# Optimization experiments

Measured on AMD Instinct MI355X. Metric: run time of the kernel, lower is better.

The kernel has to match this reference:

```python
import jax, jax.numpy as jnp
import numpy as np

B = 4096
V = 778        # MANO mesh vertices
NJ = 16        # kinematic joints
NC = 30        # pose PCA components
NS = 10        # shape components
NF = 1538      # faces
PARENTS = [0, 0, 1, 2, 0, 4, 5, 0, 7, 8, 0, 10, 11, 0, 13, 14]


def rodrigues(r):
    # r: [N,3] axis-angle -> [N,3,3] rotation matrix (Rodrigues formula)
    theta = jnp.sqrt(jnp.sum(r * r, axis=1) + 1e-8)      # [N]
    k = r / theta[:, None]
    zero = jnp.zeros_like(theta)
    K = jnp.stack([zero, -k[:, 2], k[:, 1],
                   k[:, 2], zero, -k[:, 0],
                   -k[:, 1], k[:, 0], zero], axis=1).reshape(-1, 3, 3)
    s = jnp.sin(theta)[:, None, None]
    c = jnp.cos(theta)[:, None, None]
    return jnp.eye(3, dtype=r.dtype) + s * K + (1.0 - c) * jnp.matmul(K, K)


def setup_inputs() -> dict:
    key = jax.random.key(0)
    ks = jax.random.split(key, 11)
    rot = 0.2 * jax.random.normal(ks[0], (B, 3), jnp.float32)
    pose_params = jax.random.normal(ks[1], (B, NC), jnp.float32)
    shape_params = jax.random.normal(ks[2], (B, NS), jnp.float32)
    v_template = 0.01 * jax.random.normal(ks[3], (V, 3), jnp.float32)
    shapedirs = 0.01 * jax.random.normal(ks[4], (V, 3, NS), jnp.float32)
    posedirs = 0.001 * jax.random.normal(ks[5], (V, 3, (NJ - 1) * 9), jnp.float32)
    jr = jax.random.uniform(ks[6], (NJ, V), jnp.float32)
    J_regressor = jr / jnp.sum(jr, axis=1, keepdims=True)
    w = jax.random.uniform(ks[7], (V, NJ), jnp.float32)
    weights = w / jnp.sum(w, axis=1, keepdims=True)
    hands_components = 0.1 * jax.random.normal(ks[8], (NC, (NJ - 1) * 3), jnp.float32)
    hands_mean = 0.05 * jax.random.normal(ks[9], ((NJ - 1) * 3,), jnp.float32)
    faces = jax.random.randint(ks[10], (NF, 3), 0, V)
    return dict(rot=rot, pose_params=pose_params, shape_params=shape_params,
                v_template=v_template, shapedirs=shapedirs, posedirs=posedirs,
                J_regressor=J_regressor, weights=weights,
                hands_components=hands_components, hands_mean=hands_mean,
                faces=faces)


def mano_forward(rot, pose_params, shape_params, v_template, shapedirs,
                 posedirs, J_regressor, weights, hands_components, hands_mean):
    b = rot.shape[0]
    # full pose: root rotation + PCA-decoded finger poses
    poses = (hands_mean[None, :] + pose_params @ hands_components).reshape(b, NJ - 1, 3)
    poses = jnp.concatenate([rot[:, None, :], poses], axis=1)         # [B,16,3]
    # shape blendshapes
    v_shaped = v_template[None] + jnp.einsum('bs,vcs->bvc', shape_params, shapedirs)
    # per-joint rotations and pose blendshapes (R - I for non-root joints)
    R = rodrigues(poses.reshape(-1, 3)).reshape(b, NJ, 3, 3)
    pw = (R[:, 1:] - jnp.eye(3, dtype=R.dtype)).reshape(b, (NJ - 1) * 9)
    v_posed = v_shaped + jnp.einsum('vcp,bp->bvc', posedirs, pw)
    Jp = jnp.einsum('jv,bvc->bjc', J_regressor, v_shaped)              # [B,16,3]

    def make_A(Ri, t):  # [B,3,3],[B,3] -> [B,4,4]
        top = jnp.concatenate([Ri, t[:, :, None]], axis=2)
        bot = jnp.broadcast_to(jnp.array([[[0., 0., 0., 1.]]], Ri.dtype), (b, 1, 4))
        return jnp.concatenate([top, bot], axis=1)

    # forward kinematics along the tree (16 fixed joints)
    A = [make_A(R[:, 0], Jp[:, 0])]
    for i in range(1, NJ):
        p = PARENTS[i]
        A.append(jnp.matmul(A[p], make_A(R[:, i], Jp[:, i] - Jp[:, p])))
    A_global = jnp.stack(A, axis=1)                                    # [B,16,4,4]
    # subtract transformed rest-joint locations (last column only)
    jh = jnp.concatenate([Jp, jnp.zeros((b, NJ, 1), Jp.dtype)], axis=2)
    d = jnp.einsum('bjxy,bjy->bjx', A_global, jh)
    A_rel = A_global.at[:, :, :, 3].add(-d)
    # linear blend skinning
    T = jnp.einsum('bjxy,vj->bxyv', A_rel, weights)                    # [B,4,4,V]
    rest = jnp.concatenate([v_posed, jnp.ones((b, V, 1), v_posed.dtype)], axis=2)
    v = jnp.einsum('bxyv,bvy->bxv', T, rest)                           # [B,4,V]
    # 21 joints: 16 FK joints + 5 fingertip vertices (original insert order)
    Jtr = [A_global[:, i, :3, 3:4] for i in range(NJ)]
    for pos, vid in [(4, 320), (8, 443), (12, 672), (16, 555), (20, 744)]:
        Jtr.insert(pos, v[:, :3, vid:vid + 1])
    Jtr = jnp.concatenate(Jtr, axis=2).transpose(0, 2, 1)              # [B,21,3]
    verts = v[:, :3, :].transpose(0, 2, 1)                             # [B,778,3]
    return jnp.concatenate([Jtr, verts], axis=1), poses                # [B,799,3]


def reference(rot, pose_params, shape_params, v_template, shapedirs, posedirs,
              J_regressor, weights, hands_components, hands_mean, faces):
    jv, poses = mano_forward(rot, pose_params, shape_params, v_template,
                             shapedirs, posedirs, J_regressor, weights,
                             hands_components, hands_mean)
    faces_b = jnp.broadcast_to(faces[None], (rot.shape[0],) + faces.shape)
    return jv, faces_b, poses
```

## Files before the change

### kernel.cpp

```cpp
#include <hip/hip_runtime.h>
#include <hip/hip_bf16.h>
#include <math.h>

#define NB 4096
#define NV 778
#define NJ 16
#define NC 30
#define NS 10
#define NF 1538
#define VC3 (NV*3)
#define JVROW (799*3)
#define KPAD 160
#define NPAD 2496
#define FROW (NF*3)

#define OUT_JV    0
#define OUT_FACES (NB*799*3)
#define OUT_POSES (OUT_FACES + NB*NF*3)

#define WS_JT   0
#define WS_JS   48
#define WS_AR   528
#define WA_BYTES 3147840
#define WB_BYTES 4458560

typedef __attribute__((ext_vector_type(8))) short bf16x8;
typedef __attribute__((ext_vector_type(4))) float f32x4;

__device__ const int d_pos16[16] = {0,1,2,3,5,6,7,9,10,11,13,14,15,17,18,19};

__global__ __launch_bounds__(256) void k_prep(const float* __restrict__ jr,
                                              const float* __restrict__ vt,
                                              const float* __restrict__ sd,
                                              const float* __restrict__ pdin,
                                              float* __restrict__ ws,
                                              __hip_bfloat16* __restrict__ WB)
{
    int blk = blockIdx.x;
    if (blk < 132) {
        int w = (blk * 256 + threadIdx.x) >> 6;
        int lane = threadIdx.x & 63;
        if (w >= 528) return;
        float acc = 0.f;
        if (w < 48) {
            int j = w / 3, c = w % 3;
            for (int v = lane; v < NV; v += 64) acc += jr[j*NV + v] * vt[v*3 + c];
        } else {
            int q = w - 48;
            int j = q / 30, rem = q % 30, c = rem / 10, s = rem % 10;
            for (int v = lane; v < NV; v += 64) acc += jr[j*NV + v] * sd[v*30 + c*10 + s];
        }
        for (int off = 32; off; off >>= 1) acc += __shfl_down(acc, off);
        if (lane == 0) ws[w] = acc;
    } else {
        int idx = (blk - 132) * 256 + threadIdx.x;
        if (idx >= NPAD * KPAD) return;
        int row = idx / KPAD, k = idx % KPAD;
        float val = 0.f;
        if (row < VC3) {
            if (k < 135) val = pdin[(size_t)row*135 + k];
            else if (k < 145) { int v = row/3, c = row%3; val = sd[v*30 + c*10 + (k-135)]; }
            else if (k == 145) val = vt[row];
        }
        WB[idx] = __float2bfloat16(val);
    }
}

__global__ __launch_bounds__(64) void k_batch(const float* __restrict__ rot,
                                              const float* __restrict__ pp,
                                              const float* __restrict__ sp,
                                              const float* __restrict__ hc,
                                              const float* __restrict__ hm,
                                              const int* __restrict__ faces,
                                              float* __restrict__ ws,
                                              float* __restrict__ out)
{
    __shared__ float poses_s[48];
    __shared__ float R_s[16][9];
    __shared__ float Jp_s[48];
    __shared__ float A_s[16][12];
    float* ar_ws = ws + WS_AR;
    __hip_bfloat16* WA = (__hip_bfloat16*)((char*)ws + WA_BYTES);

    int b = blockIdx.x, t = threadIdx.x;

    if (t < 3) poses_s[t] = rot[b*3 + t];
    if (t < 45) {
        float a = hm[t];
        for (int s = 0; s < NC; s++) a += pp[b*NC + s] * hc[s*45 + t];
        poses_s[3 + t] = a;
    }
    __syncthreads();
    if (t < 48) out[OUT_POSES + (size_t)b*48 + t] = poses_s[t];

    {
        float* fo = out + OUT_FACES + (size_t)b * FROW;
        for (int i = t; i < FROW/2; i += 64) {
            float2 val;
            val.x = (float)faces[2*i];
            val.y = (float)faces[2*i + 1];
            *reinterpret_cast<float2*>(fo + 2*i) = val;
        }
    }

    if (t < 48) {
        float a = ws[WS_JT + t];
        const float* js = ws + WS_JS + t*10;
        float acc = a;
        for (int s = 0; s < NS; s++) acc += js[s] * sp[b*NS + s];
        Jp_s[t] = acc;
    }
    if (t < 16) {
        float x = poses_s[t*3], y = poses_s[t*3+1], z = poses_s[t*3+2];
        float th = sqrtf(x*x + y*y + z*z + 1e-8f);
        float kx = x/th, ky = y/th, kz = z/th;
        float s = sinf(th), c = cosf(th), oc = 1.f - c;
        float* R = R_s[t];
        R[0] = 1.f + oc*(-(ky*ky + kz*kz));
        R[1] = -s*kz + oc*(kx*ky);
        R[2] =  s*ky + oc*(kx*kz);
        R[3] =  s*kz + oc*(kx*ky);
        R[4] = 1.f + oc*(-(kx*kx + kz*kz));
        R[5] = -s*kx + oc*(ky*kz);
        R[6] = -s*ky + oc*(kx*kz);
        R[7] =  s*kx + oc*(ky*kz);
        R[8] = 1.f + oc*(-(kx*kx + ky*ky));
    }
    __syncthreads();

    for (int i = t; i < KPAD; i += 64) {
        float val;
        if (i < 135) {
            int j = 1 + i/9, e = i % 9;
            val = R_s[j][e] - ((e == 0 || e == 4 || e == 8) ? 1.f : 0.f);
        } else if (i < 145) val = sp[b*NS + (i - 135)];
        else if (i == 145) val = 1.0f;
        else val = 0.f;
        WA[(size_t)b*KPAD + i] = __float2bfloat16(val);
    }

    if (t < 12) {
        int r = t >> 2, c = t & 3;
        A_s[0][t] = (c < 3) ? R_s[0][r*3 + c] : Jp_s[r];
    }
    __syncthreads();
    const int par[16] = {0,0,1,2,0,4,5,0,7,8,0,10,11,0,13,14};
    #pragma unroll
    for (int i = 1; i < 16; i++) {
        int p = par[i];
        if (t < 12) {
            int r = t >> 2, c = t & 3;
            float val;
            if (c < 3) {
                val = A_s[p][r*4+0]*R_s[i][0*3+c]
                    + A_s[p][r*4+1]*R_s[i][1*3+c]
                    + A_s[p][r*4+2]*R_s[i][2*3+c];
            } else {
                float t0 = Jp_s[i*3+0] - Jp_s[p*3+0];
                float t1 = Jp_s[i*3+1] - Jp_s[p*3+1];
                float t2 = Jp_s[i*3+2] - Jp_s[p*3+2];
                val = A_s[p][r*4+0]*t0 + A_s[p][r*4+1]*t1
                    + A_s[p][r*4+2]*t2 + A_s[p][r*4+3];
            }
            A_s[i][t] = val;
        }
        __syncthreads();
    }

    if (t < 48) {
        int j = t / 3, r = t % 3;
        out[OUT_JV + (size_t)b*JVROW + d_pos16[j]*3 + r] = A_s[j][r*4 + 3];
    }
    for (int i = t; i < 192; i += 64) {
        int j = i / 12, rc = i % 12, r = rc >> 2, c = rc & 3;
        float val = A_s[j][r*4 + c];
        if (c == 3) {
            val -= A_s[j][r*4+0]*Jp_s[j*3+0]
                 + A_s[j][r*4+1]*Jp_s[j*3+1]
                 + A_s[j][r*4+2]*Jp_s[j*3+2];
        }
        ar_ws[(size_t)b*192 + i] = val;
    }
}

__global__ __launch_bounds__(512, 6) void k_gemm_lbs(const ushort* __restrict__ WA,
                                                     const ushort* __restrict__ WB,
                                                     const float* __restrict__ ar,
                                                     const float* __restrict__ wts,
                                                     float* __restrict__ out)
{
    __shared__ __align__(16) float Cs[64][196];

    int bid = blockIdx.x;
    int swz = (bid & 7) * 104 + (bid >> 3);
    int bx = swz % 13, by = swz / 13;
    int n0 = bx * 192, b0 = by * 64;

    int tid = threadIdx.x;
    int wv = __builtin_amdgcn_readfirstlane(tid >> 6);
    int lane = tid & 63;
    int wm = wv >> 2;
    int wn = wv & 3;
    int l15 = lane & 15, lk = (lane >> 4) * 8;

    const ushort* Abase = WA + (size_t)(b0 + wm*32 + l15)*KPAD + lk;
    const ushort* Bbase = WB + (size_t)(n0 + wn*48 + l15)*KPAD + lk;

    f32x4 acc[2][3] = {};
    #pragma unroll
    for (int ks = 0; ks < 5; ks++) {
        bf16x8 a[2], bf[3];
        #pragma unroll
        for (int mi = 0; mi < 2; mi++)
            a[mi] = *(const bf16x8*)(Abase + (size_t)mi*16*KPAD + ks*32);
        #pragma unroll
        for (int ni = 0; ni < 3; ni++)
            bf[ni] = *(const bf16x8*)(Bbase + (size_t)ni*16*KPAD + ks*32);
        #pragma unroll
        for (int mi = 0; mi < 2; mi++)
            #pragma unroll
            for (int ni = 0; ni < 3; ni++)
                acc[mi][ni] = __builtin_amdgcn_mfma_f32_16x16x32_bf16(a[mi], bf[ni], acc[mi][ni], 0, 0, 0);
    }

    #pragma unroll
    for (int mi = 0; mi < 2; mi++)
        #pragma unroll
        for (int ni = 0; ni < 3; ni++)
            #pragma unroll
            for (int r = 0; r < 4; r++)
                Cs[wm*32 + mi*16 + 4*(lane>>4) + r][wn*48 + ni*16 + l15] = acc[mi][ni][r];
    __syncthreads();

    int vloc = lane;
    int v = bx*64 + vloc;
    bool vok = (v < NV);
    float w16[16];
    if (vok) {
        #pragma unroll
        for (int j = 0; j < 16; j++) w16[j] = wts[(size_t)v*16 + j];
    } else {
        #pragma unroll
        for (int j = 0; j < 16; j++) w16[j] = 0.f;
    }

    int fp = (v == 320) ? 4 : (v == 443) ? 8 : (v == 672) ? 12
           : (v == 555) ? 16 : (v == 744) ? 20 : -1;

    for (int bi = 0; bi < 8; bi++) {
        int bloc = wv*8 + bi;
        int b = b0 + bloc;
        const float* arb = ar + (size_t)b * 192;
        float x = Cs[bloc][3*vloc + 0];
        float y = Cs[bloc][3*vloc + 1];
        float z = Cs[bloc][3*vloc + 2];
        float m[12];
        #pragma unroll
        for (int k = 0; k < 12; k++) m[k] = 0.f;
        #pragma unroll
        for (int j = 0; j < 16; j++) {
            float wj = w16[j];
            #pragma unroll
            for (int k = 0; k < 12; k++) m[k] += wj * arb[j*12 + k];
        }
        if (vok) {
            float o0 = m[0]*x + m[1]*y + m[2]*z  + m[3];
            float o1 = m[4]*x + m[5]*y + m[6]*z  + m[7];
            float o2 = m[8]*x + m[9]*y + m[10]*z + m[11];
            size_t base = OUT_JV + (size_t)b*JVROW + (size_t)(21 + v)*3;
            out[base + 0] = o0; out[base + 1] = o1; out[base + 2] = o2;
            if (fp >= 0) {
                size_t jb = OUT_JV + (size_t)b*JVROW + (size_t)fp*3;
                out[jb + 0] = o0; out[jb + 1] = o1; out[jb + 2] = o2;
            }
        }
    }
}

extern "C" void kernel_launch(void* const* d_in, const int* in_sizes, int n_in,
                              void* d_out, int out_size, void* d_ws, size_t ws_size,
                              hipStream_t stream)
{
    const float* rot  = (const float*)d_in[0];
    const float* pp   = (const float*)d_in[1];
    const float* sp   = (const float*)d_in[2];
    const float* vt   = (const float*)d_in[3];
    const float* sd   = (const float*)d_in[4];
    const float* pdir = (const float*)d_in[5];
    const float* jr   = (const float*)d_in[6];
    const float* wts  = (const float*)d_in[7];
    const float* hc   = (const float*)d_in[8];
    const float* hm   = (const float*)d_in[9];
    const int*   faces= (const int*)d_in[10];
    float* out = (float*)d_out;
    float* ws  = (float*)d_ws;

    const ushort* WA = (const ushort*)((char*)d_ws + WA_BYTES);
    const ushort* WB = (const ushort*)((char*)d_ws + WB_BYTES);

    k_prep<<<132 + (NPAD*KPAD + 255)/256, 256, 0, stream>>>(jr, vt, sd, pdir, ws,
                (__hip_bfloat16*)((char*)d_ws + WB_BYTES));
    k_batch<<<NB, 64, 0, stream>>>(rot, pp, sp, hc, hm, faces, ws, out);
    k_gemm_lbs<<<13 * (NB/64), 512, 0, stream>>>(WA, WB, ws + WS_AR, wts, out);
}
```

Baseline: 71.00 us.

## Shrink GEMM-LBS batch tile to 16 and use nontemporal stores for faces

The fused GEMM+skinning kernel drops its batch tile from 64 to 16 rows and its block from 512 to 256 threads. Each wave now computes one 16x48 MFMA strip and skins 4 batch items instead of 8, with a padded LDS tile and an adjusted swizzle for 4x more blocks. The aim is better occupancy and load balance, at the cost of re-reading the B matrix for more blocks. The faces broadcast copy also switches from float2 stores to scalar nontemporal stores to avoid polluting the cache.

```diff
diff --git a/kernel.cpp b/kernel.cpp
--- a/kernel.cpp
+++ b/kernel.cpp
@@ -13,6 +13,7 @@
 #define KPAD 160
 #define NPAD 2496
 #define FROW (NF*3)
+#define BT 16
 
 #define OUT_JV    0
 #define OUT_FACES (NB*799*3)
@@ -96,10 +97,8 @@
     {
         float* fo = out + OUT_FACES + (size_t)b * FROW;
         for (int i = t; i < FROW/2; i += 64) {
-            float2 val;
-            val.x = (float)faces[2*i];
-            val.y = (float)faces[2*i + 1];
-            *reinterpret_cast<float2*>(fo + 2*i) = val;
+            __builtin_nontemporal_store((float)faces[2*i],     fo + 2*i);
+            __builtin_nontemporal_store((float)faces[2*i + 1], fo + 2*i + 1);
         }
     }
 
@@ -183,53 +182,46 @@
     }
 }
 
-__global__ __launch_bounds__(512, 6) void k_gemm_lbs(const ushort* __restrict__ WA,
+__global__ __launch_bounds__(256, 6) void k_gemm_lbs(const ushort* __restrict__ WA,
                                                      const ushort* __restrict__ WB,
                                                      const float* __restrict__ ar,
                                                      const float* __restrict__ wts,
                                                      float* __restrict__ out)
 {
-    __shared__ __align__(16) float Cs[64][196];
+    __shared__ __align__(16) float Cs[BT][197];
 
     int bid = blockIdx.x;
-    int swz = (bid & 7) * 104 + (bid >> 3);
+    int swz = (bid & 7) * 416 + (bid >> 3);
     int bx = swz % 13, by = swz / 13;
-    int n0 = bx * 192, b0 = by * 64;
+    int n0 = bx * 192, b0 = by * BT;
 
     int tid = threadIdx.x;
     int wv = __builtin_amdgcn_readfirstlane(tid >> 6);
     int lane = tid & 63;
-    int wm = wv >> 2;
-    int wn = wv & 3;
+    int wn = wv;
     int l15 = lane & 15, lk = (lane >> 4) * 8;
 
-    const ushort* Abase = WA + (size_t)(b0 + wm*32 + l15)*KPAD + lk;
+    const ushort* Abase = WA + (size_t)(b0 + l15)*KPAD + lk;
     const ushort* Bbase = WB + (size_t)(n0 + wn*48 + l15)*KPAD + lk;
 
-    f32x4 acc[2][3] = {};
+    f32x4 acc[3] = {};
     #pragma unroll
     for (int ks = 0; ks < 5; ks++) {
-        bf16x8 a[2], bf[3];
-        #pragma unroll
-        for (int mi = 0; mi < 2; mi++)
-            a[mi] = *(const bf16x8*)(Abase + (size_t)mi*16*KPAD + ks*32);
+        bf16x8 a, bf[3];
+        a = *(const bf16x8*)(Abase + ks*32);
         #pragma unroll
         for (int ni = 0; ni < 3; ni++)
             bf[ni] = *(const bf16x8*)(Bbase + (size_t)ni*16*KPAD + ks*32);
         #pragma unroll
-        for (int mi = 0; mi < 2; mi++)
-            #pragma unroll
-            for (int ni = 0; ni < 3; ni++)
-                acc[mi][ni] = __builtin_amdgcn_mfma_f32_16x16x32_bf16(a[mi], bf[ni], acc[mi][ni], 0, 0, 0);
+        for (int ni = 0; ni < 3; ni++)
+            acc[ni] = __builtin_amdgcn_mfma_f32_16x16x32_bf16(a, bf[ni], acc[ni], 0, 0, 0);
     }
 
     #pragma unroll
-    for (int mi = 0; mi < 2; mi++)
-        #pragma unroll
-        for (int ni = 0; ni < 3; ni++)
-            #pragma unroll
-            for (int r = 0; r < 4; r++)
-                Cs[wm*32 + mi*16 + 4*(lane>>4) + r][wn*48 + ni*16 + l15] = acc[mi][ni][r];
+    for (int ni = 0; ni < 3; ni++)
+        #pragma unroll
+        for (int r = 0; r < 4; r++)
+            Cs[4*(lane>>4) + r][wn*48 + ni*16 + l15] = acc[ni][r];
     __syncthreads();
 
     int vloc = lane;
@@ -247,8 +239,9 @@
     int fp = (v == 320) ? 4 : (v == 443) ? 8 : (v == 672) ? 12
            : (v == 555) ? 16 : (v == 744) ? 20 : -1;
 
-    for (int bi = 0; bi < 8; bi++) {
-        int bloc = wv*8 + bi;
+    #pragma unroll 2
+    for (int bi = 0; bi < 4; bi++) {
+        int bloc = wv*4 + bi;
         int b = b0 + bloc;
         const float* arb = ar + (size_t)b * 192;
         float x = Cs[bloc][3*vloc + 0];
@@ -301,5 +294,5 @@
     k_prep<<<132 + (NPAD*KPAD + 255)/256, 256, 0, stream>>>(jr, vt, sd, pdir, ws,
                 (__hip_bfloat16*)((char*)d_ws + WB_BYTES));
     k_batch<<<NB, 64, 0, stream>>>(rot, pp, sp, hc, hm, faces, ws, out);
-    k_gemm_lbs<<<13 * (NB/64), 512, 0, stream>>>(WA, WB, ws + WS_AR, wts, out);
-}
+    k_gemm_lbs<<<13 * (NB/BT), 256, 0, stream>>>(WA, WB, ws + WS_AR, wts, out);
+}
```

Result: slower. 73.50 us (+3.5%).
